# Performance work log

Hardware: AMD Instinct MI355X
Metric: run time of the kernel (lower is better)

## Reference

```python
import jax, jax.numpy as jnp
import numpy as np

NEG_SLOPE = 0.2
EPS = 1e-16

N_NODES = 100000
N_EDGES = 1600000
CHANNELS = 128
M_LAYERS = 3


def setup_inputs() -> dict:
    key = jax.random.key(0)
    k1, k2, k3, k4, k5 = jax.random.split(key, 5)
    x = jax.random.normal(k1, (N_NODES, CHANNELS), dtype=jnp.float32)
    edge_index = jax.random.randint(k2, (2, N_EDGES), 0, N_NODES, dtype=jnp.int64)
    # Glorot-ish scaled params, stacked over layers
    Ws = jax.random.normal(k3, (M_LAYERS, CHANNELS, CHANNELS), dtype=jnp.float32) / np.sqrt(CHANNELS)
    att_src = jax.random.normal(k4, (M_LAYERS, CHANNELS), dtype=jnp.float32) / np.sqrt(CHANNELS)
    att_dst = jax.random.normal(k5, (M_LAYERS, CHANNELS), dtype=jnp.float32) / np.sqrt(CHANNELS)
    bias = jnp.zeros((M_LAYERS, CHANNELS), dtype=jnp.float32)
    return {"x": x, "edge_index": edge_index, "Ws": Ws, "att_src": att_src,
            "att_dst": att_dst, "bias": bias}


def _gat_conv(x, src, dst, W, a_src, a_dst, b, n_nodes):
    # single-head PyG GATConv (heads=1, concat) with self-loops already in src/dst
    h = x @ W                                   # [N, C]
    s = h @ a_src                               # [N] per-node source score
    d = h @ a_dst                               # [N] per-node dest score
    e = s[src] + d[dst]                         # [E]
    e = jnp.where(e > 0, e, NEG_SLOPE * e)      # LeakyReLU(0.2)
    # segment softmax over edges grouped by destination node
    e_max = jax.ops.segment_max(e, dst, num_segments=n_nodes)
    e_max = jnp.where(jnp.isfinite(e_max), e_max, 0.0)
    w = jnp.exp(e - e_max[dst])                 # [E]
    denom = jax.ops.segment_sum(w, dst, num_segments=n_nodes)
    alpha = w / (denom[dst] + EPS)              # [E]
    out = jax.ops.segment_sum(alpha[:, None] * h[src], dst, num_segments=n_nodes)
    return out + b


def reference(x, edge_index, Ws, att_src, att_dst, bias):
    n = x.shape[0]
    loop = jnp.arange(n, dtype=edge_index.dtype)
    src = jnp.concatenate([edge_index[0], loop])   # add self loops (PyG default)
    dst = jnp.concatenate([edge_index[1], loop])
    for m in range(Ws.shape[0]):
        x = x + jax.nn.sigmoid(
            _gat_conv(x, src, dst, Ws[m], att_src[m], att_dst[m], bias[m], n))
    return x
```

## Files before the change

kernel.cpp:

```cpp
#include <hip/hip_runtime.h>
#include <hip/hip_bf16.h>
#include <math.h>

#define CH 128
#define LAYERS 3
#define NEG_SLOPE 0.2f
#define EPS_D 1e-16f
#define NBUCK_MAX 512
#define BIN_CHUNK 8192
#define PAIR_STRIDE 4608

typedef __attribute__((ext_vector_type(8))) short bf16x8;
typedef __attribute__((ext_vector_type(4))) short s16x4;
typedef __attribute__((ext_vector_type(4))) float f32x4;
typedef __attribute__((ext_vector_type(2))) float f32x2;

__device__ __forceinline__ float leaky(float e) { return e > 0.f ? e : NEG_SLOPE * e; }
__device__ __forceinline__ float sigm(float x) { return 1.f / (1.f + __expf(-x)); }

__device__ __forceinline__ unsigned bf16rne(float f) {
    unsigned u = __float_as_uint(f);
    return (u + 0x7fffu + ((u >> 16) & 1u)) >> 16;
}
__device__ __forceinline__ unsigned pack2(float f0, float f1) {
    return bf16rne(f0) | (bf16rne(f1) << 16);
}
__device__ __forceinline__ float bflo(unsigned u) { return __uint_as_float(u << 16); }
__device__ __forceinline__ float bfhi_raw(unsigned u) { return __uint_as_float(u); }

__global__ void init_bcur_k(int* __restrict__ bcursor, int nbuck) {
    int b = blockIdx.x * 256 + threadIdx.x;
    if (b < nbuck) bcursor[b] = b * PAIR_STRIDE;
}

__global__ __launch_bounds__(256) void bin_k(const int* __restrict__ EI,
                                             int* __restrict__ bcursor,
                                             unsigned* __restrict__ pairs,
                                             int ne, int nbuck) {
    __shared__ int hist[NBUCK_MAX];
    __shared__ int base[NBUCK_MAX];
    const int t = threadIdx.x;
    const int e0 = blockIdx.x * BIN_CHUNK;
    const int e1 = min(e0 + BIN_CHUNK, ne);

    for (int i = t; i < nbuck; i += 256) hist[i] = 0;
    __syncthreads();
    for (int e = e0 + t; e < e1; e += 256)
        atomicAdd(&hist[EI[ne + e] >> 8], 1);
    __syncthreads();
    for (int i = t; i < nbuck; i += 256) {
        int c = hist[i];
        base[i] = (c > 0) ? atomicAdd(&bcursor[i], c) : 0;
        hist[i] = 0;
    }
    __syncthreads();
    for (int e = e0 + t; e < e1; e += 256) {
        int src = EI[e], dst = EI[ne + e];
        int b = dst >> 8;
        int off = atomicAdd(&hist[b], 1);
        pairs[base[b] + off] = ((unsigned)src << 8) | (unsigned)(dst & 255);
    }
}

__global__ __launch_bounds__(64) void bucket_scan_k(const int* __restrict__ bcursor,
                                                    int* __restrict__ bucket_base, int nbuck) {
    const int lane = threadIdx.x;
    int carry = 0;
    for (int base = 0; base < nbuck; base += 64) {
        int b = base + lane;
        int v = (b < nbuck) ? (bcursor[b] - b * PAIR_STRIDE) : 0;
        int sc = v;
#pragma unroll
        for (int off = 1; off < 64; off <<= 1) {
            int x = __shfl_up(sc, off);
            if (lane >= off) sc += x;
        }
        if (b < nbuck) bucket_base[b] = carry + sc - v;
        carry += __shfl(sc, 63);
    }
    if (lane == 0) bucket_base[nbuck] = carry;
}

__global__ __launch_bounds__(256) void bscat_k(const int* __restrict__ bucket_base,
                                               const unsigned* __restrict__ pairs,
                                               int* __restrict__ col,
                                               int* __restrict__ rowptr, int n) {
    __shared__ int hist[256];
    __shared__ int cur[256];
    __shared__ int wsum[4];
    const int b = blockIdx.x;
    const int node0 = b << 8;
    const int t = threadIdx.x;
    const int lane = t & 63, w = t >> 6;

    hist[t] = 0;
    __syncthreads();
    const int bstart = bucket_base[b];
    const int tot = bucket_base[b + 1] - bstart;
    const int pbase = b * PAIR_STRIDE;
    for (int i = t; i < tot; i += 256)
        atomicAdd(&hist[pairs[pbase + i] & 255u], 1);
    __syncthreads();

    int v = hist[t];
    int sc = v;
#pragma unroll
    for (int off = 1; off < 64; off <<= 1) {
        int x = __shfl_up(sc, off);
        if (lane >= off) sc += x;
    }
    if (lane == 63) wsum[w] = sc;
    __syncthreads();
    if (t == 0) {
        int a = 0;
#pragma unroll
        for (int j = 0; j < 4; j++) { int tmp = wsum[j]; wsum[j] = a; a += tmp; }
    }
    __syncthreads();
    int excl = sc - v + wsum[w];
    int node = node0 + t;
    int rp = bstart + excl;
    if (node < n) {
        rowptr[node] = rp;
        cur[t] = rp;
        if (node == n - 1) rowptr[n] = rp + v;
    }
    __syncthreads();

    for (int i = t; i < tot; i += 256) {
        unsigned p = pairs[pbase + i];
        int pos = atomicAdd(&cur[p & 255u], 1);
        col[pos] = (int)(p >> 8);
    }
}

__global__ __launch_bounds__(512) void gemm_k(const float* __restrict__ X,
                                              const float* __restrict__ Wm,
                                              const float* __restrict__ asrc,
                                              const float* __restrict__ adst,
                                              unsigned* __restrict__ Hb,
                                              unsigned* __restrict__ Hf8,
                                              float* __restrict__ s,
                                              float* __restrict__ d, int n) {
    __shared__ short WT[128 * 132];
    const int t = threadIdx.x;
    const int node0 = blockIdx.x * 128;

    unsigned* WT32 = (unsigned*)WT;
#pragma unroll
    for (int i = 0; i < 16; i++) {
        int item = i * 512 + t;
        int c = item & 127, k2 = item >> 7;
        float va = Wm[(2 * k2) * 128 + c];
        float vb = Wm[(2 * k2 + 1) * 128 + c];
        WT32[c * 66 + k2] = pack2(va, vb);
    }
    __syncthreads();

    const int lane = t & 63, w = t >> 6;
    const int lr = lane & 15, lg = lane >> 4;
    const int row = w * 16 + lr;
    const int node = node0 + row;
    const int nodeA = min(node, n - 1);
    const float* xrow = X + (size_t)nodeA * CH;

    f32x4 acc[8];
#pragma unroll
    for (int ct = 0; ct < 8; ct++) acc[ct] = (f32x4){0.f, 0.f, 0.f, 0.f};

#pragma unroll
    for (int kt = 0; kt < 4; kt++) {
        const int kb = kt * 32 + lg * 8;
        const float4 fa = *(const float4*)&xrow[kb];
        const float4 fb = *(const float4*)&xrow[kb + 4];
        bf16x8 a;
        a[0] = (short)bf16rne(fa.x); a[1] = (short)bf16rne(fa.y);
        a[2] = (short)bf16rne(fa.z); a[3] = (short)bf16rne(fa.w);
        a[4] = (short)bf16rne(fb.x); a[5] = (short)bf16rne(fb.y);
        a[6] = (short)bf16rne(fb.z); a[7] = (short)bf16rne(fb.w);
#pragma unroll
        for (int ct = 0; ct < 8; ct++) {
            const int cc = ct * 16 + lr;
            s16x4 b0 = *(s16x4*)&WT[cc * 132 + kb];
            s16x4 b1 = *(s16x4*)&WT[cc * 132 + kb + 4];
            bf16x8 bb = {b0[0], b0[1], b0[2], b0[3], b1[0], b1[1], b1[2], b1[3]};
            acc[ct] = __builtin_amdgcn_mfma_f32_16x16x32_bf16(a, bb, acc[ct], 0, 0, 0);
        }
    }

    float asv[8], adv[8];
#pragma unroll
    for (int ct = 0; ct < 8; ct++) { asv[ct] = asrc[ct * 16 + lr]; adv[ct] = adst[ct * 16 + lr]; }

#pragma unroll
    for (int r = 0; r < 4; r++) {
        const int orow = w * 16 + lg * 4 + r;
        const int onode = node0 + orow;
        float ps = 0.f, pd = 0.f;
#pragma unroll
        for (int ct = 0; ct < 8; ct++) {
            float hv = acc[ct][r];
            ps += hv * asv[ct];
            pd += hv * adv[ct];
        }
        if (onode < n) {
            uint4 p;
            p.x = pack2(acc[0][r], acc[1][r]);
            p.y = pack2(acc[2][r], acc[3][r]);
            p.z = pack2(acc[4][r], acc[5][r]);
            p.w = pack2(acc[6][r], acc[7][r]);
            *(uint4*)&Hb[(size_t)onode * 64 + lr * 4] = p;
            int w0 = __builtin_amdgcn_cvt_pk_fp8_f32(acc[0][r], acc[1][r], 0, false);
            w0 = __builtin_amdgcn_cvt_pk_fp8_f32(acc[2][r], acc[3][r], w0, true);
            int w1 = __builtin_amdgcn_cvt_pk_fp8_f32(acc[4][r], acc[5][r], 0, false);
            w1 = __builtin_amdgcn_cvt_pk_fp8_f32(acc[6][r], acc[7][r], w1, true);
            uint2 q8; q8.x = (unsigned)w0; q8.y = (unsigned)w1;
            *(uint2*)&Hf8[(size_t)onode * 32 + lr * 2] = q8;
        }
#pragma unroll
        for (int off = 8; off >= 1; off >>= 1) {
            ps += __shfl_xor(ps, off);
            pd += __shfl_xor(pd, off);
        }
        if (lr == 0 && onode < n) { s[onode] = ps; d[onode] = pd; }
    }
}

__global__ __launch_bounds__(256) void node_aggr_k(const int* __restrict__ rowptr,
                                                   const int* __restrict__ col,
                                                   const float* __restrict__ s,
                                                   const float* __restrict__ d,
                                                   const unsigned* __restrict__ Hb,
                                                   const unsigned* __restrict__ Hf8,
                                                   const float* __restrict__ bias,
                                                   const float* __restrict__ x_prev,
                                                   float* __restrict__ x_next, int n) {
    long g = (long)blockIdx.x * 256 + threadIdx.x;
    int node = (int)(g >> 4);
    if (node >= n) return;
    const int tid = threadIdx.x;
    const int sub = tid & 15;
    const int qbase = tid & 48;

    const int beg = rowptr[node], end = rowptr[node + 1];
    const float dn = d[node];
    const float ev_self = leaky(s[node] + dn);

    float m = ev_self;
    float l = 0.f;
    float o[8];
#pragma unroll
    for (int k = 0; k < 8; k++) o[k] = 0.f;

    for (int j0 = beg; j0 < end; j0 += 16) {
        int cnt = min(16, end - j0);
        int srcv = 0;
        float ev = -INFINITY;
        if (sub < cnt) {
            srcv = col[j0 + sub];
            ev = leaky(s[srcv] + dn);
        }
        float bmax = ev;
#pragma unroll
        for (int off = 8; off >= 1; off >>= 1) bmax = fmaxf(bmax, __shfl_xor(bmax, off));
        float newm = fmaxf(m, bmax);
        float scale = __expf(m - newm);
        l *= scale;
#pragma unroll
        for (int k = 0; k < 8; k++) o[k] *= scale;
        m = newm;
        float wv = (sub < cnt) ? __expf(ev - m) : 0.f;

        for (int j = 0; j < cnt; j += 4) {
            int i1 = min(j + 1, cnt - 1), i2 = min(j + 2, cnt - 1), i3 = min(j + 3, cnt - 1);
            int se0 = __shfl(srcv, qbase + j);
            int se1 = __shfl(srcv, qbase + i1);
            int se2 = __shfl(srcv, qbase + i2);
            int se3 = __shfl(srcv, qbase + i3);
            float w0 = __shfl(wv, qbase + j);
            float w1 = __shfl(wv, qbase + i1);
            float w2 = __shfl(wv, qbase + i2);
            float w3 = __shfl(wv, qbase + i3);
            w1 = (j + 1 < cnt) ? w1 : 0.f;
            w2 = (j + 2 < cnt) ? w2 : 0.f;
            w3 = (j + 3 < cnt) ? w3 : 0.f;
            const uint2 u0 = *(const uint2*)&Hf8[(size_t)se0 * 32 + sub * 2];
            const uint2 u1 = *(const uint2*)&Hf8[(size_t)se1 * 32 + sub * 2];
            const uint2 u2 = *(const uint2*)&Hf8[(size_t)se2 * 32 + sub * 2];
            const uint2 u3 = *(const uint2*)&Hf8[(size_t)se3 * 32 + sub * 2];
            l += w0 + w1 + w2 + w3;
            {
                f32x2 p0 = __builtin_amdgcn_cvt_pk_f32_fp8(u0.x, false);
                f32x2 p1 = __builtin_amdgcn_cvt_pk_f32_fp8(u0.x, true);
                f32x2 p2 = __builtin_amdgcn_cvt_pk_f32_fp8(u0.y, false);
                f32x2 p3 = __builtin_amdgcn_cvt_pk_f32_fp8(u0.y, true);
                o[0] += w0 * p0[0]; o[1] += w0 * p0[1];
                o[2] += w0 * p1[0]; o[3] += w0 * p1[1];
                o[4] += w0 * p2[0]; o[5] += w0 * p2[1];
                o[6] += w0 * p3[0]; o[7] += w0 * p3[1];
            }
            {
                f32x2 p0 = __builtin_amdgcn_cvt_pk_f32_fp8(u1.x, false);
                f32x2 p1 = __builtin_amdgcn_cvt_pk_f32_fp8(u1.x, true);
                f32x2 p2 = __builtin_amdgcn_cvt_pk_f32_fp8(u1.y, false);
                f32x2 p3 = __builtin_amdgcn_cvt_pk_f32_fp8(u1.y, true);
                o[0] += w1 * p0[0]; o[1] += w1 * p0[1];
                o[2] += w1 * p1[0]; o[3] += w1 * p1[1];
                o[4] += w1 * p2[0]; o[5] += w1 * p2[1];
                o[6] += w1 * p3[0]; o[7] += w1 * p3[1];
            }
            {
                f32x2 p0 = __builtin_amdgcn_cvt_pk_f32_fp8(u2.x, false);
                f32x2 p1 = __builtin_amdgcn_cvt_pk_f32_fp8(u2.x, true);
                f32x2 p2 = __builtin_amdgcn_cvt_pk_f32_fp8(u2.y, false);
                f32x2 p3 = __builtin_amdgcn_cvt_pk_f32_fp8(u2.y, true);
                o[0] += w2 * p0[0]; o[1] += w2 * p0[1];
                o[2] += w2 * p1[0]; o[3] += w2 * p1[1];
                o[4] += w2 * p2[0]; o[5] += w2 * p2[1];
                o[6] += w2 * p3[0]; o[7] += w2 * p3[1];
            }
            {
                f32x2 p0 = __builtin_amdgcn_cvt_pk_f32_fp8(u3.x, false);
                f32x2 p1 = __builtin_amdgcn_cvt_pk_f32_fp8(u3.x, true);
                f32x2 p2 = __builtin_amdgcn_cvt_pk_f32_fp8(u3.y, false);
                f32x2 p3 = __builtin_amdgcn_cvt_pk_f32_fp8(u3.y, true);
                o[0] += w3 * p0[0]; o[1] += w3 * p0[1];
                o[2] += w3 * p1[0]; o[3] += w3 * p1[1];
                o[4] += w3 * p2[0]; o[5] += w3 * p2[1];
                o[6] += w3 * p3[0]; o[7] += w3 * p3[1];
            }
        }
    }

    float wself = __expf(ev_self - m);
    l += wself;
    const uint4 us = *(const uint4*)&Hb[(size_t)node * 64 + sub * 4];
    o[0] += wself * bflo(us.x);
    o[1] += wself * bfhi_raw(us.x);
    o[2] += wself * bflo(us.y);
    o[3] += wself * bfhi_raw(us.y);
    o[4] += wself * bflo(us.z);
    o[5] += wself * bfhi_raw(us.z);
    o[6] += wself * bflo(us.w);
    o[7] += wself * bfhi_raw(us.w);

    float inv = 1.f / (l + EPS_D);
    const long rowb = (long)node * CH;
#pragma unroll
    for (int k = 0; k < 8; k++) {
        int c = k * 16 + sub;
        float r = x_prev[rowb + c] + sigm(o[k] * inv + bias[c]);
        x_next[rowb + c] = r;
    }
}

extern "C" void kernel_launch(void* const* d_in, const int* in_sizes, int n_in,
                              void* d_out, int out_size, void* d_ws, size_t ws_size,
                              hipStream_t stream) {
    const float* x_in = (const float*)d_in[0];
    const int* EI = (const int*)d_in[1];
    const float* Ws_all = (const float*)d_in[2];
    const float* asrc_all = (const float*)d_in[3];
    const float* adst_all = (const float*)d_in[4];
    const float* bias_all = (const float*)d_in[5];
    float* out = (float*)d_out;

    const int n = in_sizes[0] / CH;
    const int ne = in_sizes[1] / 2;
    const long NC = (long)n * CH;
    const int nbuck = (n + 255) >> 8;

    unsigned* hb = (unsigned*)d_ws;
    unsigned* hf8 = hb + NC / 2;
    float* s = (float*)(hf8 + NC / 4);
    float* dd = s + n;
    float* x_ws = dd + n;
    int* rowptr = (int*)(x_ws + NC);
    int* bucket_base = rowptr + (n + 1);
    int* bcursor = bucket_base + (nbuck + 1);
    int* colv = bcursor + nbuck;
    unsigned* pairs = (unsigned*)(colv + ne);

    init_bcur_k<<<(nbuck + 255) / 256, 256, 0, stream>>>(bcursor, nbuck);
    bin_k<<<(ne + BIN_CHUNK - 1) / BIN_CHUNK, 256, 0, stream>>>(EI, bcursor, pairs, ne, nbuck);
    bucket_scan_k<<<1, 64, 0, stream>>>(bcursor, bucket_base, nbuck);
    bscat_k<<<nbuck, 256, 0, stream>>>(bucket_base, pairs, colv, rowptr, n);

    const float* xp[LAYERS] = {x_in, out, x_ws};
    float* xn[LAYERS] = {out, x_ws, out};

    for (int m = 0; m < LAYERS; m++) {
        const float* Wm = Ws_all + (size_t)m * CH * CH;
        const float* as = asrc_all + (size_t)m * CH;
        const float* ad = adst_all + (size_t)m * CH;
        const float* bm = bias_all + (size_t)m * CH;

        gemm_k<<<(n + 127) / 128, 512, 0, stream>>>(xp[m], Wm, as, ad, hb, hf8, s, dd, n);
        node_aggr_k<<<((long)n * 16 + 255) / 256, 256, 0, stream>>>(rowptr, colv, s, dd, hb, hf8,
                                                                    bm, xp[m], xn[m], n);
    }
}
```

Baseline: 258.4 us.

## Sort nodes by degree for aggregation and drop global bucket scan

```diff
diff --git a/kernel.cpp b/kernel.cpp
--- a/kernel.cpp
+++ b/kernel.cpp
@@ -9,6 +9,7 @@
 #define NBUCK_MAX 512
 #define BIN_CHUNK 8192
 #define PAIR_STRIDE 4608
+#define DBINS 64
 
 typedef __attribute__((ext_vector_type(8))) short bf16x8;
 typedef __attribute__((ext_vector_type(4))) short s16x4;
@@ -27,11 +28,6 @@
 }
 __device__ __forceinline__ float bflo(unsigned u) { return __uint_as_float(u << 16); }
 __device__ __forceinline__ float bfhi_raw(unsigned u) { return __uint_as_float(u); }
-
-__global__ void init_bcur_k(int* __restrict__ bcursor, int nbuck) {
-    int b = blockIdx.x * 256 + threadIdx.x;
-    if (b < nbuck) bcursor[b] = b * PAIR_STRIDE;
-}
 
 __global__ __launch_bounds__(256) void bin_k(const int* __restrict__ EI,
                                              int* __restrict__ bcursor,
@@ -50,7 +46,7 @@
     __syncthreads();
     for (int i = t; i < nbuck; i += 256) {
         int c = hist[i];
-        base[i] = (c > 0) ? atomicAdd(&bcursor[i], c) : 0;
+        base[i] = (c > 0) ? (i * PAIR_STRIDE + atomicAdd(&bcursor[i], c)) : 0;
         hist[i] = 0;
     }
     __syncthreads();
@@ -62,29 +58,11 @@
     }
 }
 
-__global__ __launch_bounds__(64) void bucket_scan_k(const int* __restrict__ bcursor,
-                                                    int* __restrict__ bucket_base, int nbuck) {
-    const int lane = threadIdx.x;
-    int carry = 0;
-    for (int base = 0; base < nbuck; base += 64) {
-        int b = base + lane;
-        int v = (b < nbuck) ? (bcursor[b] - b * PAIR_STRIDE) : 0;
-        int sc = v;
-#pragma unroll
-        for (int off = 1; off < 64; off <<= 1) {
-            int x = __shfl_up(sc, off);
-            if (lane >= off) sc += x;
-        }
-        if (b < nbuck) bucket_base[b] = carry + sc - v;
-        carry += __shfl(sc, 63);
-    }
-    if (lane == 0) bucket_base[nbuck] = carry;
-}
-
-__global__ __launch_bounds__(256) void bscat_k(const int* __restrict__ bucket_base,
+__global__ __launch_bounds__(256) void bscat_k(const int* __restrict__ bcursor,
                                                const unsigned* __restrict__ pairs,
                                                int* __restrict__ col,
-                                               int* __restrict__ rowptr, int n) {
+                                               int* __restrict__ rowbeg,
+                                               int* __restrict__ rowend, int n) {
     __shared__ int hist[256];
     __shared__ int cur[256];
     __shared__ int wsum[4];
@@ -95,9 +73,8 @@
 
     hist[t] = 0;
     __syncthreads();
-    const int bstart = bucket_base[b];
-    const int tot = bucket_base[b + 1] - bstart;
     const int pbase = b * PAIR_STRIDE;
+    const int tot = bcursor[b];
     for (int i = t; i < tot; i += 256)
         atomicAdd(&hist[pairs[pbase + i] & 255u], 1);
     __syncthreads();
@@ -119,11 +96,11 @@
     __syncthreads();
     int excl = sc - v + wsum[w];
     int node = node0 + t;
-    int rp = bstart + excl;
+    int rp = pbase + excl;
     if (node < n) {
-        rowptr[node] = rp;
+        rowbeg[node] = rp;
+        rowend[node] = rp + v;
         cur[t] = rp;
-        if (node == n - 1) rowptr[n] = rp + v;
     }
     __syncthreads();
 
@@ -131,6 +108,64 @@
         unsigned p = pairs[pbase + i];
         int pos = atomicAdd(&cur[p & 255u], 1);
         col[pos] = (int)(p >> 8);
+    }
+}
+
+__global__ __launch_bounds__(256) void dhist_k(const int* __restrict__ rowbeg,
+                                               const int* __restrict__ rowend,
+                                               int* __restrict__ dtot, int n) {
+    __shared__ int hist[DBINS];
+    const int t = threadIdx.x;
+    const int n0 = blockIdx.x * 1024;
+    const int n1 = min(n0 + 1024, n);
+    if (t < DBINS) hist[t] = 0;
+    __syncthreads();
+    for (int i = n0 + t; i < n1; i += 256)
+        atomicAdd(&hist[min(rowend[i] - rowbeg[i], DBINS - 1)], 1);
+    __syncthreads();
+    if (t < DBINS) {
+        int c = hist[t];
+        if (c > 0) atomicAdd(&dtot[t], c);
+    }
+}
+
+__global__ __launch_bounds__(64) void dscan_k(const int* __restrict__ dtot,
+                                              int* __restrict__ dcur) {
+    const int lane = threadIdx.x;
+    int v = dtot[lane];
+    int sc = v;
+#pragma unroll
+    for (int off = 1; off < 64; off <<= 1) {
+        int x = __shfl_up(sc, off);
+        if (lane >= off) sc += x;
+    }
+    dcur[lane] = sc - v;
+}
+
+__global__ __launch_bounds__(256) void dsort_k(const int* __restrict__ rowbeg,
+                                               const int* __restrict__ rowend,
+                                               int* __restrict__ dcur,
+                                               int* __restrict__ order, int n) {
+    __shared__ int hist[DBINS];
+    __shared__ int base[DBINS];
+    const int t = threadIdx.x;
+    const int n0 = blockIdx.x * 1024;
+    const int n1 = min(n0 + 1024, n);
+    if (t < DBINS) hist[t] = 0;
+    __syncthreads();
+    for (int i = n0 + t; i < n1; i += 256)
+        atomicAdd(&hist[min(rowend[i] - rowbeg[i], DBINS - 1)], 1);
+    __syncthreads();
+    if (t < DBINS) {
+        int c = hist[t];
+        base[t] = (c > 0) ? atomicAdd(&dcur[t], c) : 0;
+        hist[t] = 0;
+    }
+    __syncthreads();
+    for (int i = n0 + t; i < n1; i += 256) {
+        int bn = min(rowend[i] - rowbeg[i], DBINS - 1);
+        int off = atomicAdd(&hist[bn], 1);
+        order[base[bn] + off] = i;
     }
 }
 
@@ -226,7 +261,9 @@
     }
 }
 
-__global__ __launch_bounds__(256) void node_aggr_k(const int* __restrict__ rowptr,
+__global__ __launch_bounds__(256) void node_aggr_k(const int* __restrict__ order,
+                                                   const int* __restrict__ rowbeg,
+                                                   const int* __restrict__ rowend,
                                                    const int* __restrict__ col,
                                                    const float* __restrict__ s,
                                                    const float* __restrict__ d,
@@ -236,13 +273,14 @@
                                                    const float* __restrict__ x_prev,
                                                    float* __restrict__ x_next, int n) {
     long g = (long)blockIdx.x * 256 + threadIdx.x;
-    int node = (int)(g >> 4);
-    if (node >= n) return;
+    int nidx = (int)(g >> 4);
+    if (nidx >= n) return;
+    const int node = order[nidx];
     const int tid = threadIdx.x;
     const int sub = tid & 15;
     const int qbase = tid & 48;
 
-    const int beg = rowptr[node], end = rowptr[node + 1];
+    const int beg = rowbeg[node], end = rowend[node];
     const float dn = d[node];
     const float ev_self = leaky(s[node] + dn);
 
@@ -369,22 +407,28 @@
     const int ne = in_sizes[1] / 2;
     const long NC = (long)n * CH;
     const int nbuck = (n + 255) >> 8;
+    const int nsb = (n + 1023) / 1024;
 
     unsigned* hb = (unsigned*)d_ws;
     unsigned* hf8 = hb + NC / 2;
     float* s = (float*)(hf8 + NC / 4);
     float* dd = s + n;
     float* x_ws = dd + n;
-    int* rowptr = (int*)(x_ws + NC);
-    int* bucket_base = rowptr + (n + 1);
-    int* bcursor = bucket_base + (nbuck + 1);
-    int* colv = bcursor + nbuck;
-    unsigned* pairs = (unsigned*)(colv + ne);
-
-    init_bcur_k<<<(nbuck + 255) / 256, 256, 0, stream>>>(bcursor, nbuck);
+    int* rowbeg = (int*)(x_ws + NC);
+    int* rowend = rowbeg + n;
+    int* order = rowend + n;
+    int* bcursor = order + n;
+    int* dtot = bcursor + nbuck;
+    int* dcur = dtot + DBINS;
+    int* colv = dcur + DBINS;
+    unsigned* pairs = (unsigned*)(colv + nbuck * PAIR_STRIDE);
+
+    hipMemsetAsync(bcursor, 0, (size_t)(nbuck + 2 * DBINS) * sizeof(int), stream);
     bin_k<<<(ne + BIN_CHUNK - 1) / BIN_CHUNK, 256, 0, stream>>>(EI, bcursor, pairs, ne, nbuck);
-    bucket_scan_k<<<1, 64, 0, stream>>>(bcursor, bucket_base, nbuck);
-    bscat_k<<<nbuck, 256, 0, stream>>>(bucket_base, pairs, colv, rowptr, n);
+    bscat_k<<<nbuck, 256, 0, stream>>>(bcursor, pairs, colv, rowbeg, rowend, n);
+    dhist_k<<<nsb, 256, 0, stream>>>(rowbeg, rowend, dtot, n);
+    dscan_k<<<1, 64, 0, stream>>>(dtot, dcur);
+    dsort_k<<<nsb, 256, 0, stream>>>(rowbeg, rowend, dcur, order, n);
 
     const float* xp[LAYERS] = {x_in, out, x_ws};
     float* xn[LAYERS] = {out, x_ws, out};
@@ -396,7 +440,8 @@
         const float* bm = bias_all + (size_t)m * CH;
 
         gemm_k<<<(n + 127) / 128, 512, 0, stream>>>(xp[m], Wm, as, ad, hb, hf8, s, dd, n);
-        node_aggr_k<<<((long)n * 16 + 255) / 256, 256, 0, stream>>>(rowptr, colv, s, dd, hb, hf8,
-                                                                    bm, xp[m], xn[m], n);
-    }
-}
+        node_aggr_k<<<((long)n * 16 + 255) / 256, 256, 0, stream>>>(order, rowbeg, rowend, colv,
+                                                                    s, dd, hb, hf8, bm,
+                                                                    xp[m], xn[m], n);
+    }
+}
```

After: 278.0 us. +7.6%, slower.
